# Optimization experiments

Hardware: AMD Instinct MI355X
Metric: run time of the kernel (lower is better)

## Reference

```python
import jax, jax.numpy as jnp
import numpy as np

D_MODEL = 1024
N_HEADS = 16
SEQ_LEN = 2048
BATCH = 2
NEG = -1.0e9


def sinusoidal_embeddings(seq_len, d_k):
    # Faithful to the torch version: row 0 is all zeros; even cols get sin,
    # odd cols get cos of position/theta (theta uses the SAME index j, not j//2).
    theta = 10000.0 ** (2.0 * jnp.arange(d_k, dtype=jnp.float32) / d_k)  # [d_k]
    pos = jnp.arange(1, seq_len, dtype=jnp.float32)[:, None] / theta      # [S-1, d_k]
    even = (jnp.arange(d_k) % 2 == 0)
    body = jnp.where(even, jnp.sin(pos), jnp.cos(pos))                    # [S-1, d_k]
    return jnp.concatenate([jnp.zeros((1, d_k), dtype=pos.dtype), body], axis=0)


def setup_inputs() -> dict:
    key = jax.random.key(0)
    k_x, k_q, k_k, k_v, k_o = jax.random.split(key, 5)
    scale = 0.02
    return {
        "X": jax.random.normal(k_x, (BATCH, SEQ_LEN, D_MODEL), dtype=jnp.float32),
        "W_q": jax.random.normal(k_q, (D_MODEL, D_MODEL), dtype=jnp.float32) * scale,
        "W_k": jax.random.normal(k_k, (D_MODEL, D_MODEL), dtype=jnp.float32) * scale,
        "W_v": jax.random.normal(k_v, (D_MODEL, D_MODEL), dtype=jnp.float32) * scale,
        "W_o": jax.random.normal(k_o, (D_MODEL, D_MODEL), dtype=jnp.float32) * scale,
    }


def reference(X, W_q, W_k, W_v, W_o):
    B, S, D = X.shape
    H, d_k = N_HEADS, D // N_HEADS

    def proj(W):  # nn.Linear (no bias): y = x @ W.T, then split heads -> [B,H,S,d_k]
        return (X @ W.T).reshape(B, S, H, d_k).transpose(0, 2, 1, 3)

    Q, K, V = proj(W_q), proj(W_k), proj(W_v)

    pos = sinusoidal_embeddings(S, d_k)          # [S, d_k]
    Q = Q + pos
    K = K + pos

    mask = jnp.triu(jnp.full((S, S), NEG, dtype=X.dtype), k=1)  # [S,S]
    scores = jnp.einsum("bhqd,bhkd->bhqk", Q, K) / jnp.sqrt(jnp.float32(d_k)) + mask
    weights = jax.nn.softmax(scores, axis=-1)
    attn = jnp.einsum("bhqk,bhkd->bhqd", weights, V)            # [B,H,S,d_k]

    attn = attn.transpose(0, 2, 1, 3).reshape(B, S, D)
    return attn @ W_o.T + X
```

## Files before the change

### kernel.cpp

```cpp
#include <hip/hip_runtime.h>
#include <hip/hip_bf16.h>
#include <math.h>

#define S_LEN 2048
#define DMODEL 1024
#define NHEADS 16
#define DHEAD 64
#define NBATCH 2
#define MROWS (NBATCH * S_LEN)

typedef float f32x4 __attribute__((ext_vector_type(4)));
typedef unsigned short u16x8 __attribute__((ext_vector_type(8)));
typedef __bf16 bf16x8 __attribute__((ext_vector_type(8)));

__device__ __forceinline__ f32x4 mfma16(u16x8 a, u16x8 b, f32x4 c) {
    return __builtin_amdgcn_mfma_f32_16x16x32_bf16(
        __builtin_bit_cast(bf16x8, a), __builtin_bit_cast(bf16x8, b), c, 0, 0, 0);
}

__device__ __forceinline__ unsigned short f2bf(float f) {
    unsigned int u = __builtin_bit_cast(unsigned int, f);
    u += 0x7FFFu + ((u >> 16) & 1u);
    return (unsigned short)(u >> 16);
}

__device__ __forceinline__ unsigned int cvtpk(float lo, float hi) {
    unsigned int r;
    asm("v_cvt_pk_bf16_f32 %0, %1, %2" : "=v"(r) : "v"(lo), "v"(hi));
    return r;
}

__device__ __forceinline__ void gl16(const void* g, void* l) {
    __builtin_amdgcn_global_load_lds(
        (const __attribute__((address_space(1))) unsigned int*)g,
        (__attribute__((address_space(3))) unsigned int*)l, 16, 0, 0);
}

#define PIPE_BAR_12() do { \
    asm volatile("s_waitcnt vmcnt(12)" ::: "memory"); \
    __builtin_amdgcn_sched_barrier(0); \
    __builtin_amdgcn_s_barrier(); \
    __builtin_amdgcn_sched_barrier(0); } while (0)
#define PIPE_BAR_6() do { \
    asm volatile("s_waitcnt vmcnt(6)" ::: "memory"); \
    __builtin_amdgcn_sched_barrier(0); \
    __builtin_amdgcn_s_barrier(); \
    __builtin_amdgcn_sched_barrier(0); } while (0)
#define PIPE_BAR_0() do { \
    asm volatile("s_waitcnt vmcnt(0)" ::: "memory"); \
    __builtin_amdgcn_sched_barrier(0); \
    __builtin_amdgcn_s_barrier(); \
    __builtin_amdgcn_sched_barrier(0); } while (0)

__global__ __launch_bounds__(256) void cvt5(
    const float* __restrict__ X, const float* __restrict__ Wq,
    const float* __restrict__ Wk, const float* __restrict__ Wv,
    const float* __restrict__ Wo,
    unsigned short* __restrict__ Xbf, unsigned short* __restrict__ Wbf,
    float* __restrict__ pos)
{
    int b = blockIdx.x;
    if (b >= 4096) {
        int i = (b - 4096) * 256 + threadIdx.x;
        int s = i >> 6, d = i & 63;
        float theta = powf(10000.0f, (2.0f * (float)d) / 64.0f);
        float x = (float)s / theta;
        float v = (d & 1) ? cosf(x) : sinf(x);
        pos[i] = (s == 0) ? 0.0f : v;
        return;
    }
    const float* s; unsigned short* d; int t;
    if (b < 2048) { s = X; d = Xbf; t = b * 256 + threadIdx.x; }
    else {
        int z = (b - 2048) >> 9, bb = (b - 2048) & 511;
        s = (z == 0) ? Wq : (z == 1) ? Wk : (z == 2) ? Wv : Wo;
        d = Wbf + (z << 20);
        t = bb * 256 + threadIdx.x;
    }
    float4 a = *((const float4*)s + t * 2);
    float4 c = *((const float4*)s + t * 2 + 1);
    u16x8 o;
    o[0] = f2bf(a.x); o[1] = f2bf(a.y); o[2] = f2bf(a.z); o[3] = f2bf(a.w);
    o[4] = f2bf(c.x); o[5] = f2bf(c.y); o[6] = f2bf(c.z); o[7] = f2bf(c.w);
    *((u16x8*)d + t) = o;
}

__global__ __launch_bounds__(128) void gemm_qkv(
    const unsigned short* __restrict__ Xbf, const unsigned short* __restrict__ Wbf,
    const float* __restrict__ pos,
    unsigned short* __restrict__ qb, unsigned short* __restrict__ kb,
    unsigned short* __restrict__ vt)
{
    const int y = blockIdx.y;
    const int z = y >> 4;
    const unsigned short* __restrict__ W = Wbf + (z << 20);
    __shared__ unsigned short L[3][6144];
    const int t = threadIdx.x;
    const int lane = t & 63;
    const int w = t >> 6;
    const int m0 = blockIdx.x * 128;
    const int n0 = (y & 15) * 64;
    const int ll = lane & 15, lg = lane >> 4;
    const int r16 = lane >> 2, c4 = lane & 3;
    const int swzr = (r16 & 3) ^ ((r16 >> 2) & 3);
    const int swzll = (ll & 3) ^ ((ll >> 2) & 3);

    f32x4 acc[4][4] = {};

    const unsigned short* gA[4];
    const unsigned short* gB[2];
    #pragma unroll
    for (int i = 0; i < 4; i++)
        gA[i] = Xbf + (m0 + w * 64 + i * 16 + r16) * 1024 + ((c4 ^ swzr) * 8);
    #pragma unroll
    for (int i = 0; i < 2; i++)
        gB[i] = W + (n0 + w * 32 + i * 16 + r16) * 1024 + ((c4 ^ swzr) * 8);

    const int sw = ((lg ^ swzll) & 3) * 16;

    auto stage = [&](unsigned short* Lb) {
        unsigned short* const dA = Lb + w * 2048;
        unsigned short* const dB = Lb + 4096 + w * 1024;
        #pragma unroll
        for (int i = 0; i < 4; i++) { gl16(gA[i], dA + i * 512); gA[i] += 32; }
        #pragma unroll
        for (int i = 0; i < 2; i++) { gl16(gB[i], dB + i * 512); gB[i] += 32; }
    };
    auto compute = [&](const unsigned short* Lb) {
        const char* const pA = (const char*)Lb + (w * 64 + ll) * 64 + sw;
        const char* const pB = (const char*)Lb + 8192 + ll * 64 + sw;
        u16x8 af[4], bfv[4];
        #pragma unroll
        for (int m = 0; m < 4; m++) af[m] = *(const u16x8*)(pA + m * 1024);
        #pragma unroll
        for (int n = 0; n < 4; n++) bfv[n] = *(const u16x8*)(pB + n * 1024);
        __builtin_amdgcn_s_setprio(1);
        #pragma unroll
        for (int m = 0; m < 4; m++)
            #pragma unroll
            for (int n = 0; n < 4; n++)
                acc[m][n] = mfma16(af[m], bfv[n], acc[m][n]);
        __builtin_amdgcn_s_setprio(0);
    };

    stage(L[0]);
    stage(L[1]);
    PIPE_BAR_6();
    for (int tt = 0; tt < 10; tt++) {
        stage(L[2]); compute(L[0]); PIPE_BAR_6();
        stage(L[0]); compute(L[1]); PIPE_BAR_6();
        stage(L[1]); compute(L[2]); PIPE_BAR_6();
    }
    compute(L[0]); PIPE_BAR_0();
    compute(L[1]);

    if (z == 2) {
        #pragma unroll
        for (int m = 0; m < 4; m++) {
            const int row0 = m0 + w * 64 + m * 16 + lg * 4;
            const int b = row0 >> 11, s0 = row0 & 2047;
            #pragma unroll
            for (int n = 0; n < 4; n++) {
                const int c = n0 + n * 16 + ll;
                const int h = c >> 6, d = c & 63;
                unsigned long long pk =
                    (unsigned long long)cvtpk(acc[m][n][0], acc[m][n][1]) |
                    ((unsigned long long)cvtpk(acc[m][n][2], acc[m][n][3]) << 32);
                *(unsigned long long*)&vt[(((b * NHEADS + h) * 64) + d) * S_LEN + s0] = pk;
            }
        }
    } else {
        unsigned short* const dst = (z == 0) ? qb : kb;
        #pragma unroll
        for (int m = 0; m < 4; m++) {
            #pragma unroll
            for (int n = 0; n < 4; n++) {
                #pragma unroll
                for (int r = 0; r < 4; r++) {
                    const int row = m0 + w * 64 + m * 16 + lg * 4 + r;
                    const int c = n0 + n * 16 + ll;
                    const int b = row >> 11, s = row & 2047;
                    const int h = c >> 6, d = c & 63;
                    float v = acc[m][n][r] + pos[s * 64 + d];
                    if (z == 0) v *= 0.1803368801111244f;
                    dst[(((b * NHEADS + h) * S_LEN) + s) * 64 + d] = f2bf(v);
                }
            }
        }
    }
}

__global__ __launch_bounds__(512, 4) void attn_kernel(
    const unsigned short* __restrict__ qb,
    const unsigned short* __restrict__ kb,
    const unsigned short* __restrict__ vt,
    unsigned short* __restrict__ attnb)
{
    __shared__ unsigned short Klds[2][128 * 64];
    __shared__ unsigned short Vlds[2][64 * 128];
    __shared__ unsigned short Plds[8][16 * 64];

    const int bh = blockIdx.y;
    const int x = blockIdx.x;
    const int qt = (bh < 16) ? (15 - x) : x;

    const int lane = threadIdx.x & 63;
    const int w = threadIdx.x >> 6;
    const int lg = lane >> 4, ll = lane & 15;
    const int r8 = lane >> 3, ch = (lane & 7) ^ r8;
    const int r4 = lane >> 4, c16 = lane & 15;

    const unsigned short* Q = qb + bh * (S_LEN * 64);
    const unsigned short* K = kb + bh * (S_LEN * 64);
    const unsigned short* V = vt + bh * (64 * S_LEN);
    const int q0 = qt * 128 + w * 16;

    u16x8 qf0 = *(const u16x8*)(Q + (q0 + ll) * 64 + lg * 8);
    u16x8 qf1 = *(const u16x8*)(Q + (q0 + ll) * 64 + 32 + lg * 8);

    f32x4 o_acc[4] = {};
    float l_part = 0.0f;

    const int sw0 = ((0 * 4 + lg) ^ (ll & 7)) * 16;
    const int sw1 = ((1 * 4 + lg) ^ (ll & 7)) * 16;
    const char* kb0p0 = (const char*)&Klds[0][0] + ll * 128 + sw0;
    const char* kb0p1 = (const char*)&Klds[0][0] + ll * 128 + sw1;
    const char* kb1p0 = (const char*)&Klds[1][0] + ll * 128 + sw0;
    const char* kb1p1 = (const char*)&Klds[1][0] + ll * 128 + sw1;
    const char* vb0p0 = (const char*)&Vlds[0][0] + ll * 256 + sw0;
    const char* vb0p1 = (const char*)&Vlds[0][0] + ll * 256 + sw1;
    const char* vb1p0 = (const char*)&Vlds[1][0] + ll * 256 + sw0;
    const char* vb1p1 = (const char*)&Vlds[1][0] + ll * 256 + sw1;
    const int E = (ll & 7) << 4;
    char* pwb = (char*)&Plds[w][0] + (((ll * 128) + lg * 8) ^ (E & 16));
    const int pw_o0 = 0 ^ (E & 96), pw_o1 = 32 ^ (E & 96);
    const int pw_o2 = 64 ^ (E & 96), pw_o3 = 96 ^ (E & 96);
    const char* pr0 = (const char*)&Plds[w][0] + ll * 128 + sw0;
    const char* pr1 = (const char*)&Plds[w][0] + ll * 128 + sw1;
    unsigned short* kd0 = &Klds[0][(w * 16) * 64];
    unsigned short* kd1 = &Klds[1][(w * 16) * 64];
    unsigned short* vd0 = &Vlds[0][(w * 8) * 128];
    unsigned short* vd1 = &Vlds[1][(w * 8) * 128];
    const unsigned short* gk  = K + (w * 16 + r8) * 64 + ch * 8;
    const unsigned short* gva = V + (w * 8 + r4) * S_LEN + ((c16 ^ r4) * 8);
    const unsigned short* gvb = V + (w * 8 + 4 + r4) * S_LEN + ((c16 ^ (4 + r4)) * 8);
    const int dthr = w * 16 + ll - lg * 4;

    auto stage2 = [&](unsigned short* kd, unsigned short* vd) {
        gl16(gk, kd);
        gl16(gk + 512, kd + 512);
        gl16(gva, vd);
        gl16(gvb, vd + 512);
        gk += 128 * 64;
        gva += 128;
        gvb += 128;
    };

    auto tile_body = [&](const char* kp0, const char* kp1,
                         const char* vp0, const char* vp1, bool masked, int thr) {
        f32x4 sc[4] = {};
        __builtin_amdgcn_s_setprio(1);
        #pragma unroll
        for (int f = 0; f < 4; f++) {
            const u16x8 kfa = *(const u16x8*)(kp0 + f * 2048);
            sc[f] = mfma16(kfa, qf0, sc[f]);
            const u16x8 kfb = *(const u16x8*)(kp1 + f * 2048);
            sc[f] = mfma16(kfb, qf1, sc[f]);
        }
        __builtin_amdgcn_s_setprio(0);
        if (masked) {
            #pragma unroll
            for (int f = 0; f < 4; f++)
                #pragma unroll
                for (int r = 0; r < 4; r++)
                    if (f * 16 + r > thr) sc[f][r] = -1.0e9f;
        }
        float ts = 0.0f;
        #pragma unroll
        for (int f = 0; f < 4; f++)
            #pragma unroll
            for (int r = 0; r < 4; r++) {
                const float p = __builtin_amdgcn_exp2f(sc[f][r]);
                sc[f][r] = p;
                ts += p;
            }
        l_part += ts;
        *(unsigned long long*)(pwb + pw_o0) =
            (unsigned long long)cvtpk(sc[0][0], sc[0][1]) | ((unsigned long long)cvtpk(sc[0][2], sc[0][3]) << 32);
        *(unsigned long long*)(pwb + pw_o1) =
            (unsigned long long)cvtpk(sc[1][0], sc[1][1]) | ((unsigned long long)cvtpk(sc[1][2], sc[1][3]) << 32);
        *(unsigned long long*)(pwb + pw_o2) =
            (unsigned long long)cvtpk(sc[2][0], sc[2][1]) | ((unsigned long long)cvtpk(sc[2][2], sc[2][3]) << 32);
        *(unsigned long long*)(pwb + pw_o3) =
            (unsigned long long)cvtpk(sc[3][0], sc[3][1]) | ((unsigned long long)cvtpk(sc[3][2], sc[3][3]) << 32);
        const u16x8 pf0 = *(const u16x8*)pr0;
        const u16x8 pf1 = *(const u16x8*)pr1;
        __builtin_amdgcn_s_setprio(1);
        #pragma unroll
        for (int f = 0; f < 4; f++) {
            o_acc[f] = mfma16(pf0, *(const u16x8*)(vp0 + f * 4096), o_acc[f]);
            o_acc[f] = mfma16(pf1, *(const u16x8*)(vp1 + f * 4096), o_acc[f]);
        }
        __builtin_amdgcn_s_setprio(0);
    };

    auto body128_full = [&](const char* kp0, const char* kp1,
                            const char* vp0, const char* vp1) {
        tile_body(kp0, kp1, vp0, vp1, false, 0);
        tile_body(kp0 + 8192, kp1 + 8192, vp0 + 128, vp1 + 128, false, 0);
    };
    auto body128_diag = [&](const char* kp0, const char* kp1,
                            const char* vp0, const char* vp1) {
        tile_body(kp0, kp1, vp0, vp1, true, dthr);
        if (w >= 4)
            tile_body(kp0 + 8192, kp1 + 8192, vp0 + 128, vp1 + 128, true, dthr - 64);
    };

    stage2(kd0, vd0);
    __syncthreads();

    int p = 0;
    while (p + 2 <= qt) {
        stage2(kd1, vd1);
        body128_full(kb0p0, kb0p1, vb0p0, vb0p1);
        __syncthreads();
        stage2(kd0, vd0);
        body128_full(kb1p0, kb1p1, vb1p0, vb1p1);
        __syncthreads();
        p += 2;
    }
    if (p < qt) {
        stage2(kd1, vd1);
        body128_full(kb0p0, kb0p1, vb0p0, vb0p1);
        __syncthreads();
        body128_diag(kb1p0, kb1p1, vb1p0, vb1p1);
    } else {
        body128_diag(kb0p0, kb0p1, vb0p0, vb0p1);
    }

    l_part += __shfl_xor(l_part, 16);
    l_part += __shfl_xor(l_part, 32);

    const int bb = bh >> 4, h = bh & 15;
    float lr0 = 1.0f / __shfl(l_part, lg * 4 + 0);
    float lr1 = 1.0f / __shfl(l_part, lg * 4 + 1);
    float lr2 = 1.0f / __shfl(l_part, lg * 4 + 2);
    float lr3 = 1.0f / __shfl(l_part, lg * 4 + 3);
    #pragma unroll
    for (int f = 0; f < 4; f++) {
        const int colbase = h * 64 + f * 16 + ll;
        attnb[(bb * S_LEN + q0 + lg * 4 + 0) * DMODEL + colbase] = f2bf(o_acc[f][0] * lr0);
        attnb[(bb * S_LEN + q0 + lg * 4 + 1) * DMODEL + colbase] = f2bf(o_acc[f][1] * lr1);
        attnb[(bb * S_LEN + q0 + lg * 4 + 2) * DMODEL + colbase] = f2bf(o_acc[f][2] * lr2);
        attnb[(bb * S_LEN + q0 + lg * 4 + 3) * DMODEL + colbase] = f2bf(o_acc[f][3] * lr3);
    }
}

__global__ __launch_bounds__(128) void gemm_out(
    const unsigned short* __restrict__ Abf,
    const unsigned short* __restrict__ Wbf,
    const float* __restrict__ X,
    float* __restrict__ out)
{
    const unsigned short* __restrict__ W = Wbf + (3u << 20);
    __shared__ unsigned short L[3][192 * 64];
    const int t = threadIdx.x;
    const int lane = t & 63;
    const int w = t >> 6;
    const int m0 = blockIdx.x * 128;
    const int n0 = blockIdx.y * 64;
    const int ll = lane & 15, lg = lane >> 4;
    const int r8 = lane >> 3, ch = (lane & 7) ^ r8;

    f32x4 acc[4][4] = {};

    const unsigned short* gA[8];
    const unsigned short* gB[4];
    #pragma unroll
    for (int i = 0; i < 8; i++) gA[i] = Abf + (m0 + w * 64 + i * 8 + r8) * 1024 + ch * 8;
    #pragma unroll
    for (int i = 0; i < 4; i++) gB[i] = W + (n0 + w * 32 + i * 8 + r8) * 1024 + ch * 8;

    const int sw0 = ((0 * 4 + lg) ^ (ll & 7)) * 16;
    const int sw1 = ((1 * 4 + lg) ^ (ll & 7)) * 16;

    auto stage = [&](unsigned short* Lb) {
        unsigned short* const dA = Lb + (w * 64) * 64;
        unsigned short* const dB = Lb + 128 * 64 + (w * 32) * 64;
        #pragma unroll
        for (int i = 0; i < 8; i++) { gl16(gA[i], dA + i * 8 * 64); gA[i] += 64; }
        #pragma unroll
        for (int i = 0; i < 4; i++) { gl16(gB[i], dB + i * 8 * 64); gB[i] += 64; }
    };
    auto compute = [&](const unsigned short* Lb) {
        const char* const pA0 = (const char*)Lb + (w * 64 + ll) * 128 + sw0;
        const char* const pA1 = (const char*)Lb + (w * 64 + ll) * 128 + sw1;
        const char* const pB0 = (const char*)Lb + 16384 + ll * 128 + sw0;
        const char* const pB1 = (const char*)Lb + 16384 + ll * 128 + sw1;
        u16x8 af[4], bfv[4];
        #pragma unroll
        for (int m = 0; m < 4; m++) af[m] = *(const u16x8*)(pA0 + m * 2048);
        #pragma unroll
        for (int n = 0; n < 4; n++) bfv[n] = *(const u16x8*)(pB0 + n * 2048);
        __builtin_amdgcn_s_setprio(1);
        #pragma unroll
        for (int m = 0; m < 4; m++)
            #pragma unroll
            for (int n = 0; n < 4; n++)
                acc[m][n] = mfma16(af[m], bfv[n], acc[m][n]);
        __builtin_amdgcn_s_setprio(0);
        #pragma unroll
        for (int m = 0; m < 4; m++) af[m] = *(const u16x8*)(pA1 + m * 2048);
        #pragma unroll
        for (int n = 0; n < 4; n++) bfv[n] = *(const u16x8*)(pB1 + n * 2048);
        __builtin_amdgcn_s_setprio(1);
        #pragma unroll
        for (int m = 0; m < 4; m++)
            #pragma unroll
            for (int n = 0; n < 4; n++)
                acc[m][n] = mfma16(af[m], bfv[n], acc[m][n]);
        __builtin_amdgcn_s_setprio(0);
    };

    stage(L[0]);
    stage(L[1]);
    PIPE_BAR_12();
    for (int tt = 0; tt < 4; tt++) {
        stage(L[2]); compute(L[0]); PIPE_BAR_12();
        stage(L[0]); compute(L[1]); PIPE_BAR_12();
        stage(L[1]); compute(L[2]); PIPE_BAR_12();
    }
    stage(L[2]); compute(L[0]); PIPE_BAR_12();
    stage(L[0]); compute(L[1]); PIPE_BAR_12();
    compute(L[2]); PIPE_BAR_0();
    compute(L[0]);

    #pragma unroll
    for (int m = 0; m < 4; m++)
        #pragma unroll
        for (int n = 0; n < 4; n++)
            #pragma unroll
            for (int r = 0; r < 4; r++) {
                const int row = m0 + w * 64 + m * 16 + lg * 4 + r;
                const int col = n0 + n * 16 + ll;
                out[row * 1024 + col] = acc[m][n][r] + X[row * 1024 + col];
            }
}

extern "C" void kernel_launch(void* const* d_in, const int* in_sizes, int n_in,
                              void* d_out, int out_size, void* d_ws, size_t ws_size,
                              hipStream_t stream) {
    const float* X  = (const float*)d_in[0];
    const float* Wq = (const float*)d_in[1];
    const float* Wk = (const float*)d_in[2];
    const float* Wv = (const float*)d_in[3];
    const float* Wo = (const float*)d_in[4];
    float* out = (float*)d_out;

    char* ws = (char*)d_ws;
    float*          pos  = (float*)(ws);
    unsigned short* Xbf  = (unsigned short*)(ws + (512u << 10));
    unsigned short* Wbf  = (unsigned short*)(ws + (512u << 10) + (8u  << 20));
    unsigned short* qb   = (unsigned short*)(ws + (512u << 10) + (16u << 20));
    unsigned short* kb   = (unsigned short*)(ws + (512u << 10) + (24u << 20));
    unsigned short* vt   = (unsigned short*)(ws + (512u << 10) + (32u << 20));
    unsigned short* attb = Xbf;

    cvt5<<<dim3(4608), dim3(256), 0, stream>>>(X, Wq, Wk, Wv, Wo, Xbf, Wbf, pos);
    gemm_qkv<<<dim3(32, 48), dim3(128), 0, stream>>>(Xbf, Wbf, pos, qb, kb, vt);
    attn_kernel<<<dim3(16, 32), dim3(512), 0, stream>>>(qb, kb, vt, attb);
    gemm_out<<<dim3(32, 16), dim3(128), 0, stream>>>(attb, Wbf, X, out);
}
```

Baseline: 107.0 us.

## Enlarge QKV GEMM tiles to 256x256 with 8 waves and interleaved staging

Rewrites the QKV projection GEMM to use 256x256 output tiles per 512-thread block with K-step 64 and double-buffered LDS, instead of 128x64 tiles with 128 threads and triple buffering. Global-to-LDS loads for the next K tile are split into four chunks interleaved between MFMA quads, each chunk separated by a barrier. The aim is higher arithmetic intensity and less global traffic per FLOP. In exchange the grid shrinks to 192 blocks, which is below the CU count on MI355X, and each block uses 128KB of LDS, which limits occupancy.

```diff
diff --git a/kernel.cpp b/kernel.cpp
--- a/kernel.cpp
+++ b/kernel.cpp
@@ -38,11 +38,6 @@
 
 #define PIPE_BAR_12() do { \
     asm volatile("s_waitcnt vmcnt(12)" ::: "memory"); \
-    __builtin_amdgcn_sched_barrier(0); \
-    __builtin_amdgcn_s_barrier(); \
-    __builtin_amdgcn_sched_barrier(0); } while (0)
-#define PIPE_BAR_6() do { \
-    asm volatile("s_waitcnt vmcnt(6)" ::: "memory"); \
     __builtin_amdgcn_sched_barrier(0); \
     __builtin_amdgcn_s_barrier(); \
     __builtin_amdgcn_sched_barrier(0); } while (0)
@@ -85,103 +80,139 @@
     *((u16x8*)d + t) = o;
 }
 
-__global__ __launch_bounds__(128) void gemm_qkv(
+__global__ __launch_bounds__(512) void gemm_qkv(
     const unsigned short* __restrict__ Xbf, const unsigned short* __restrict__ Wbf,
     const float* __restrict__ pos,
     unsigned short* __restrict__ qb, unsigned short* __restrict__ kb,
     unsigned short* __restrict__ vt)
 {
     const int y = blockIdx.y;
-    const int z = y >> 4;
+    const int z = y >> 2;
     const unsigned short* __restrict__ W = Wbf + (z << 20);
-    __shared__ unsigned short L[3][6144];
+    __shared__ unsigned short L[2][32768];
     const int t = threadIdx.x;
     const int lane = t & 63;
     const int w = t >> 6;
-    const int m0 = blockIdx.x * 128;
-    const int n0 = (y & 15) * 64;
+    const int wm = w >> 2, wn = w & 3;
+    const int m0 = blockIdx.x * 256;
+    const int nb = (y & 3) * 256;
     const int ll = lane & 15, lg = lane >> 4;
-    const int r16 = lane >> 2, c4 = lane & 3;
-    const int swzr = (r16 & 3) ^ ((r16 >> 2) & 3);
-    const int swzll = (ll & 3) ^ ((ll >> 2) & 3);
-
-    f32x4 acc[4][4] = {};
+    const int tr = t >> 3;
+    const int ch = (t & 7) ^ (tr & 7);
+
+    f32x4 acc[8][4] = {};
 
     const unsigned short* gA[4];
-    const unsigned short* gB[2];
+    const unsigned short* gB[4];
     #pragma unroll
-    for (int i = 0; i < 4; i++)
-        gA[i] = Xbf + (m0 + w * 64 + i * 16 + r16) * 1024 + ((c4 ^ swzr) * 8);
-    #pragma unroll
-    for (int i = 0; i < 2; i++)
-        gB[i] = W + (n0 + w * 32 + i * 16 + r16) * 1024 + ((c4 ^ swzr) * 8);
-
-    const int sw = ((lg ^ swzll) & 3) * 16;
-
-    auto stage = [&](unsigned short* Lb) {
-        unsigned short* const dA = Lb + w * 2048;
-        unsigned short* const dB = Lb + 4096 + w * 1024;
-        #pragma unroll
-        for (int i = 0; i < 4; i++) { gl16(gA[i], dA + i * 512); gA[i] += 32; }
-        #pragma unroll
-        for (int i = 0; i < 2; i++) { gl16(gB[i], dB + i * 512); gB[i] += 32; }
-    };
-    auto compute = [&](const unsigned short* Lb) {
-        const char* const pA = (const char*)Lb + (w * 64 + ll) * 64 + sw;
-        const char* const pB = (const char*)Lb + 8192 + ll * 64 + sw;
-        u16x8 af[4], bfv[4];
-        #pragma unroll
-        for (int m = 0; m < 4; m++) af[m] = *(const u16x8*)(pA + m * 1024);
-        #pragma unroll
-        for (int n = 0; n < 4; n++) bfv[n] = *(const u16x8*)(pB + n * 1024);
+    for (int i = 0; i < 4; i++) {
+        gA[i] = Xbf + (m0 + i * 64 + tr) * 1024 + ch * 8;
+        gB[i] = W + (nb + i * 64 + tr) * 1024 + ch * 8;
+    }
+
+    const int sw0 = ((0 * 4 + lg) ^ (ll & 7)) * 16;
+    const int sw1 = ((1 * 4 + lg) ^ (ll & 7)) * 16;
+    const int aBase = (wm * 128 + ll) * 128;
+    const int bBase = 32768 + (wn * 64 + ll) * 128;
+
+    auto sqA01 = [&](unsigned short* Ln) {
+        gl16(gA[0], Ln + (0 * 64 + w * 8) * 64); gA[0] += 64;
+        gl16(gA[1], Ln + (1 * 64 + w * 8) * 64); gA[1] += 64;
+    };
+    auto sqA23 = [&](unsigned short* Ln) {
+        gl16(gA[2], Ln + (2 * 64 + w * 8) * 64); gA[2] += 64;
+        gl16(gA[3], Ln + (3 * 64 + w * 8) * 64); gA[3] += 64;
+    };
+    auto sqB01 = [&](unsigned short* Ln) {
+        gl16(gB[0], Ln + 16384 + (0 * 64 + w * 8) * 64); gB[0] += 64;
+        gl16(gB[1], Ln + 16384 + (1 * 64 + w * 8) * 64); gB[1] += 64;
+    };
+    auto sqB23 = [&](unsigned short* Ln) {
+        gl16(gB[2], Ln + 16384 + (2 * 64 + w * 8) * 64); gB[2] += 64;
+        gl16(gB[3], Ln + 16384 + (3 * 64 + w * 8) * 64); gB[3] += 64;
+    };
+
+    u16x8 bf[4][2];
+
+    auto quad = [&](int q, const char* bA) {
+        const char* pa = bA + aBase + q * 4096;
+        u16x8 a00 = *(const u16x8*)(pa + sw0);
+        u16x8 a01 = *(const u16x8*)(pa + sw1);
+        u16x8 a10 = *(const u16x8*)(pa + 2048 + sw0);
+        u16x8 a11 = *(const u16x8*)(pa + 2048 + sw1);
         __builtin_amdgcn_s_setprio(1);
         #pragma unroll
-        for (int m = 0; m < 4; m++)
-            #pragma unroll
-            for (int n = 0; n < 4; n++)
-                acc[m][n] = mfma16(af[m], bfv[n], acc[m][n]);
+        for (int nf = 0; nf < 4; nf++) {
+            acc[q * 2 + 0][nf] = mfma16(a00, bf[nf][0], acc[q * 2 + 0][nf]);
+            acc[q * 2 + 1][nf] = mfma16(a10, bf[nf][0], acc[q * 2 + 1][nf]);
+        }
+        #pragma unroll
+        for (int nf = 0; nf < 4; nf++) {
+            acc[q * 2 + 0][nf] = mfma16(a01, bf[nf][1], acc[q * 2 + 0][nf]);
+            acc[q * 2 + 1][nf] = mfma16(a11, bf[nf][1], acc[q * 2 + 1][nf]);
+        }
         __builtin_amdgcn_s_setprio(0);
     };
 
-    stage(L[0]);
-    stage(L[1]);
-    PIPE_BAR_6();
-    for (int tt = 0; tt < 10; tt++) {
-        stage(L[2]); compute(L[0]); PIPE_BAR_6();
-        stage(L[0]); compute(L[1]); PIPE_BAR_6();
-        stage(L[1]); compute(L[2]); PIPE_BAR_6();
-    }
-    compute(L[0]); PIPE_BAR_0();
-    compute(L[1]);
+    auto ktile = [&](const unsigned short* Lb, unsigned short* Ln, bool stg) {
+        const char* bA = (const char*)Lb;
+        const char* bB = (const char*)Lb;
+        if (stg) sqA01(Ln);
+        #pragma unroll
+        for (int nf = 0; nf < 4; nf++) {
+            const char* p = bB + bBase + nf * 2048;
+            bf[nf][0] = *(const u16x8*)(p + sw0);
+            bf[nf][1] = *(const u16x8*)(p + sw1);
+        }
+        quad(0, bA);
+        __builtin_amdgcn_s_barrier();
+        if (stg) sqA23(Ln);
+        quad(1, bA);
+        __builtin_amdgcn_s_barrier();
+        if (stg) sqB01(Ln);
+        quad(2, bA);
+        __builtin_amdgcn_s_barrier();
+        if (stg) sqB23(Ln);
+        quad(3, bA);
+        PIPE_BAR_0();
+    };
+
+    sqA01(L[0]); sqA23(L[0]); sqB01(L[0]); sqB23(L[0]);
+    PIPE_BAR_0();
+    #pragma unroll 1
+    for (int tt = 0; tt < 8; tt++) {
+        ktile(L[0], L[1], true);
+        ktile(L[1], L[0], tt != 7);
+    }
 
     if (z == 2) {
         #pragma unroll
-        for (int m = 0; m < 4; m++) {
-            const int row0 = m0 + w * 64 + m * 16 + lg * 4;
+        for (int mf = 0; mf < 8; mf++) {
+            const int row0 = m0 + wm * 128 + mf * 16 + lg * 4;
             const int b = row0 >> 11, s0 = row0 & 2047;
             #pragma unroll
-            for (int n = 0; n < 4; n++) {
-                const int c = n0 + n * 16 + ll;
+            for (int nf = 0; nf < 4; nf++) {
+                const int c = nb + wn * 64 + nf * 16 + ll;
                 const int h = c >> 6, d = c & 63;
                 unsigned long long pk =
-                    (unsigned long long)cvtpk(acc[m][n][0], acc[m][n][1]) |
-                    ((unsigned long long)cvtpk(acc[m][n][2], acc[m][n][3]) << 32);
+                    (unsigned long long)cvtpk(acc[mf][nf][0], acc[mf][nf][1]) |
+                    ((unsigned long long)cvtpk(acc[mf][nf][2], acc[mf][nf][3]) << 32);
                 *(unsigned long long*)&vt[(((b * NHEADS + h) * 64) + d) * S_LEN + s0] = pk;
             }
         }
     } else {
         unsigned short* const dst = (z == 0) ? qb : kb;
         #pragma unroll
-        for (int m = 0; m < 4; m++) {
-            #pragma unroll
-            for (int n = 0; n < 4; n++) {
+        for (int mf = 0; mf < 8; mf++) {
+            #pragma unroll
+            for (int nf = 0; nf < 4; nf++) {
                 #pragma unroll
                 for (int r = 0; r < 4; r++) {
-                    const int row = m0 + w * 64 + m * 16 + lg * 4 + r;
-                    const int c = n0 + n * 16 + ll;
+                    const int row = m0 + wm * 128 + mf * 16 + lg * 4 + r;
+                    const int c = nb + wn * 64 + nf * 16 + ll;
                     const int b = row >> 11, s = row & 2047;
                     const int h = c >> 6, d = c & 63;
-                    float v = acc[m][n][r] + pos[s * 64 + d];
+                    float v = acc[mf][nf][r] + pos[s * 64 + d];
                     if (z == 0) v *= 0.1803368801111244f;
                     dst[(((b * NHEADS + h) * S_LEN) + s) * 64 + d] = f2bf(v);
                 }
@@ -467,7 +498,7 @@
     unsigned short* attb = Xbf;
 
     cvt5<<<dim3(4608), dim3(256), 0, stream>>>(X, Wq, Wk, Wv, Wo, Xbf, Wbf, pos);
-    gemm_qkv<<<dim3(32, 48), dim3(128), 0, stream>>>(Xbf, Wbf, pos, qb, kb, vt);
+    gemm_qkv<<<dim3(16, 12), dim3(512), 0, stream>>>(Xbf, Wbf, pos, qb, kb, vt);
     attn_kernel<<<dim3(16, 32), dim3(512), 0, stream>>>(qb, kb, vt, attb);
     gemm_out<<<dim3(32, 16), dim3(128), 0, stream>>>(attb, Wbf, X, out);
 }
```

Measured after the change: 95.79 us. 10.5% less time.
